# Optimization experiments

Hardware: AMD Instinct MI355X
Metric: run time of the kernel (lower is better)

## Reference

```python
import jax, jax.numpy as jnp
import numpy as np

D_HEAD = 128
N_HEADS = 8
BATCH = 8
SEQ = 1024


def setup_inputs() -> dict:
    key = jax.random.key(0)
    ks = jax.random.split(key, 11)
    d, nh = D_HEAD, N_HEADS
    D = nh * d
    s_in = 1.0 / np.sqrt(d)   # torch Linear default init bound, fan_in=d
    s_out = 1.0 / np.sqrt(D)  # fan_in=D for out_proj
    u = lambda k, shape, s: jax.random.uniform(k, shape, jnp.float32, -s, s)
    return {
        "q": jax.random.normal(ks[0], (BATCH, SEQ, d), jnp.float32),
        "k": jax.random.normal(ks[1], (BATCH, SEQ, d), jnp.float32),
        "v": jax.random.normal(ks[2], (BATCH, SEQ, d), jnp.float32),
        "Wq": u(ks[3], (d, D), s_in), "bq": u(ks[4], (D,), s_in),
        "Wk": u(ks[5], (d, D), s_in), "bk": u(ks[6], (D,), s_in),
        "Wv": u(ks[7], (d, D), s_in), "bv": u(ks[8], (D,), s_in),
        "Wo": u(ks[9], (D, d), s_out), "bo": u(ks[10], (d,), s_out),
    }


def reference(q, k, v, Wq, bq, Wk, bk, Wv, bv, Wo, bo):
    B, T, d_in = q.shape
    S = k.shape[1]
    nh = N_HEADS
    # projections: [B, L, nh*d] -> [B, nh, L, d]
    split = lambda x: x.reshape(x.shape[0], x.shape[1], nh, -1).transpose(0, 2, 1, 3)
    qh = split(q @ Wq + bq)
    kh = split(k @ Wk + bk)
    vh = split(v @ Wv + bv)
    d_head = qh.shape[-1]
    # scaled dot-product scores: [B, nh, T, S]
    scores = jnp.einsum('bhtd,bhsd->bhts', qh, kh) / jnp.sqrt(jnp.float32(d_head))
    # causal mask (future positions -> -inf), matches triu(fill(-inf), 1)
    causal = jnp.triu(jnp.ones((T, S), dtype=bool), 1)
    scores = jnp.where(causal[None, None], -jnp.inf, scores)
    # softmax in float32 then cast back, as the original does
    probs = jax.nn.softmax(scores.astype(jnp.float32), axis=-1).astype(scores.dtype)
    o = jnp.einsum('bhts,bhsd->bhtd', probs, vh)          # [B, nh, T, d]
    o = o.transpose(0, 2, 1, 3).reshape(B, T, nh * d_head)  # [B, T, D]
    return o @ Wo + bo                                     # [B, T, d]
```

## Files before the change

### kernel.cpp

```cpp
#include <hip/hip_runtime.h>
#include <hip/hip_bf16.h>


typedef __attribute__((ext_vector_type(8))) short short8;
typedef __attribute__((ext_vector_type(4))) short short4v;
typedef __attribute__((ext_vector_type(4))) float f32x4;

#define B_   8
#define S_   1024
#define DH_  128
#define NH_  8
#define DM_  1024

#define MFMA16(a, b, c) __builtin_amdgcn_mfma_f32_16x16x32_bf16((a), (b), (c), 0, 0, 0)

#define GLOAD_LDS16(gsrc, ldst)                                              \
  __builtin_amdgcn_global_load_lds(                                          \
      (const __attribute__((address_space(1))) void*)(gsrc),                 \
      (__attribute__((address_space(3))) void*)(ldst), 16, 0, 0)

__device__ __forceinline__ float bf2f(unsigned short u) {
  union { unsigned int i; float f; } x; x.i = ((unsigned int)u) << 16; return x.f;
}
__device__ __forceinline__ unsigned short f2bf(float f) {
  union { float f; unsigned int i; } x; x.f = f;
  unsigned int r = (x.i + 0x7fffu + ((x.i >> 16) & 1u)) >> 16;
  return (unsigned short)r;
}
__device__ __forceinline__ unsigned short f2h(float f) {
  union { _Float16 h; unsigned short u; } x; x.h = (_Float16)f; return x.u;
}
__device__ __forceinline__ float h2f(unsigned short u) {
  union { unsigned short u; _Float16 h; } x; x.u = u; return (float)x.h;
}
__device__ __forceinline__ float ldany(const void* p, int i, int fp) {
  return fp ? ((const float*)p)[i] : bf2f(((const unsigned short*)p)[i]);
}

__global__ void k_detect(const unsigned short* __restrict__ in, int* __restrict__ flag) {
  __shared__ int f;
  int tid = threadIdx.x;
  if (tid == 0) f = 0;
  __syncthreads();
  int t = 0;
  for (int i = tid; i < 16384; i += 256) {
    unsigned h = in[i];
    unsigned e = (h >> 7) & 0xFFu, m = h & 0x7Fu;
    if (e == 0xFFu || (e == 0u && m != 0u)) t = 1;
  }
  if (t) atomicOr(&f, 1);
  __syncthreads();
  if (tid == 0) *flag = f;
}

__global__ void k_cvt_x(const void* __restrict__ q, const void* __restrict__ k,
                        const void* __restrict__ v, const int* __restrict__ flag,
                        unsigned short* __restrict__ Xq, unsigned short* __restrict__ Xk,
                        unsigned short* __restrict__ Xv) {
  const int fp = *flag;
  int z = blockIdx.y;
  const void* in = (z == 0) ? q : (z == 1) ? k : v;
  unsigned short* out = (z == 0) ? Xq : (z == 1) ? Xk : Xv;
  int e8 = (blockIdx.x * 256 + threadIdx.x) * 8;
  if (fp) {
    const float* xf = (const float*)in + e8;
    f32x4 x0 = *(const f32x4*)xf;
    f32x4 x1 = *(const f32x4*)(xf + 4);
    short8 o;
#pragma unroll
    for (int j = 0; j < 4; ++j) { o[j] = (short)f2bf(x0[j]); o[4 + j] = (short)f2bf(x1[j]); }
    *(short8*)&out[e8] = o;
  } else {
    *(short8*)&out[e8] = *(const short8*)((const unsigned short*)in + e8);
  }
}

__global__ void k_cvt_w(const void* __restrict__ Wq, const void* __restrict__ Wk,
                        const void* __restrict__ Wv, const void* __restrict__ Wo,
                        const void* __restrict__ bq, const void* __restrict__ bk,
                        const void* __restrict__ bv, const void* __restrict__ bo,
                        const int* __restrict__ flag,
                        unsigned short* __restrict__ wqT, unsigned short* __restrict__ wkT,
                        unsigned short* __restrict__ wvT, unsigned short* __restrict__ woT,
                        unsigned short* __restrict__ bqc, unsigned short* __restrict__ bkc,
                        unsigned short* __restrict__ bvc, unsigned short* __restrict__ boc) {
  const int fp = *flag;
  int g = blockIdx.x * 256 + threadIdx.x;
  if (g < 393216) {
    int z = g >> 17, e = g & 131071;
    const void* in = (z == 0) ? Wq : (z == 1) ? Wk : Wv;
    unsigned short* out = (z == 0) ? wqT : (z == 1) ? wkT : wvT;
    int r = e >> 10, c = e & 1023;
    out[c * 128 + r] = f2bf(ldany(in, e, fp));
  } else if (g < 524288) {
    int e = g - 393216;
    int r = e >> 7, c = e & 127;
    woT[c * 1024 + r] = f2bf(ldany(Wo, e, fp));
  } else if (g < 525312) {
    int e = g - 524288; bqc[e] = f2bf(ldany(bq, e, fp));
  } else if (g < 526336) {
    int e = g - 525312; bkc[e] = f2bf(ldany(bk, e, fp));
  } else if (g < 527360) {
    int e = g - 526336; bvc[e] = f2bf(ldany(bv, e, fp));
  } else if (g < 527488) {
    int e = g - 527360; boc[e] = f2bf(ldany(bo, e, fp));
  }
}

__global__ __launch_bounds__(256) void k_qkv(
    const unsigned short* __restrict__ Xq, const unsigned short* __restrict__ Xk,
    const unsigned short* __restrict__ Xv,
    const unsigned short* __restrict__ WqT, const unsigned short* __restrict__ WkT,
    const unsigned short* __restrict__ WvT,
    const unsigned short* __restrict__ bq, const unsigned short* __restrict__ bk,
    const unsigned short* __restrict__ bv,
    unsigned short* __restrict__ Qp, unsigned short* __restrict__ Kp,
    unsigned short* __restrict__ VpT) {
  __shared__ __align__(16) unsigned short vtile[128][136];

  const int mat = blockIdx.z;
  const unsigned short* X    = (mat == 0) ? Xq  : (mat == 1) ? Xk  : Xv;
  const unsigned short* WT   = (mat == 0) ? WqT : (mat == 1) ? WkT : WvT;
  const unsigned short* bias = (mat == 0) ? bq  : (mat == 1) ? bk  : bv;
  const float scale = (mat == 0) ? (1.4426950408889634f / 11.313708498984761f) : 1.0f;

  const int tid = threadIdx.x, lane = tid & 63, wave = tid >> 6;
  const int wm = wave >> 1, wn = wave & 1;
  const int l15 = lane & 15, lg = lane >> 4;
  const int mbase = blockIdx.x * 128 + wm * 64;
  const int nbase = blockIdx.y * 128 + wn * 64;

  short8 a[4][4];
#pragma unroll
  for (int mi = 0; mi < 4; ++mi)
#pragma unroll
    for (int kk = 0; kk < 4; ++kk)
      a[mi][kk] = *(const short8*)&X[(mbase + mi * 16 + l15) * DH_ + kk * 32 + lg * 8];

  f32x4 acc[4][4];
#pragma unroll
  for (int mi = 0; mi < 4; ++mi)
#pragma unroll
    for (int ni = 0; ni < 4; ++ni) acc[mi][ni] = (f32x4){0.f, 0.f, 0.f, 0.f};

  short8 bfr[2][4];
#pragma unroll
  for (int kk = 0; kk < 4; ++kk)
    bfr[0][kk] = *(const short8*)&WT[(nbase + l15) * DH_ + kk * 32 + lg * 8];

#pragma unroll
  for (int ni = 0; ni < 4; ++ni) {
    if (ni < 3) {
#pragma unroll
      for (int kk = 0; kk < 4; ++kk)
        bfr[(ni + 1) & 1][kk] =
            *(const short8*)&WT[(nbase + (ni + 1) * 16 + l15) * DH_ + kk * 32 + lg * 8];
    }
#pragma unroll
    for (int mi = 0; mi < 4; ++mi)
#pragma unroll
      for (int kk = 0; kk < 4; ++kk)
        acc[mi][ni] = MFMA16(a[mi][kk], bfr[ni & 1][kk], acc[mi][ni]);
  }

#pragma unroll
  for (int mi = 0; mi < 4; ++mi)
#pragma unroll
    for (int ni = 0; ni < 4; ++ni) {
      int nl = wn * 64 + ni * 16 + l15;
      float bv_ = bf2f(bias[blockIdx.y * 128 + nl]);
#pragma unroll
      for (int reg = 0; reg < 4; ++reg) {
        int ml_ = wm * 64 + mi * 16 + lg * 4 + reg;
        vtile[ml_][nl] = f2bf((acc[mi][ni][reg] + bv_) * scale);
      }
    }
  __syncthreads();

  const int b = blockIdx.x >> 3;
  const int h = blockIdx.y;
  if (mat < 2) {
    unsigned short* Out = ((mat == 0) ? Qp : Kp) +
        ((b * NH_ + h) * S_ + (blockIdx.x & 7) * 128) * DH_;
#pragma unroll
    for (int j = 0; j < 8; ++j) {
      int r = j * 16 + (tid >> 4);
      int c0 = (tid & 15) * 8;
      short8 v = *(const short8*)&vtile[r][c0];
      *(short8*)&Out[j * 2048 + tid * 8] = v;
    }
  } else {
    int n = tid >> 1;
    int thalf = (tid & 1) * 64;
    int base = ((b * NH_ + h) * DH_ + n) * S_ + (blockIdx.x & 7) * 128 + thalf;
#pragma unroll
    for (int jj = 0; jj < 8; ++jj) {
      short8 v;
#pragma unroll
      for (int j2 = 0; j2 < 8; ++j2) v[j2] = (short)vtile[thalf + jj * 8 + j2][n];
      *(short8*)&VpT[base + jj * 8] = v;
    }
  }
}

__global__ __launch_bounds__(256) void k_attn_split(
    const unsigned short* __restrict__ Qp, const unsigned short* __restrict__ Kp,
    const unsigned short* __restrict__ VpT,
    unsigned short* __restrict__ Opart, float* __restrict__ ml,
    unsigned short* __restrict__ O) {
  __shared__ __align__(16) unsigned short kbuf[2][4096];
  __shared__ __align__(16) unsigned short vbuf[2][4096];
  __shared__ __align__(16) unsigned short plds[4][16][44];

  const int tid = threadIdx.x, lane = tid & 63, w = tid >> 6;
  const int l15 = lane & 15, lg = lane >> 4;

  const int bid = blockIdx.x;
  const int swz = (bid & 7) * 320 + (bid >> 3);
  const int bh = swz / 40;
  const int bj = 39 - (swz % 40);
  int G, c;
  if (bj < 4)       { G = bj;                  c = 0; }
  else if (bj < 12) { G = 4 + ((bj - 4) >> 1); c = (bj - 4) & 1; }
  else if (bj < 24) { G = 8 + (bj - 12) / 3;   c = (bj - 12) % 3; }
  else              { G = 12 + ((bj - 24) >> 2); c = (bj - 24) & 3; }
  const int qw = 4 * G + w;
  const int q0 = qw * 16;
  const int cd = G >> 2;
  const bool dia = (c == cd);
  const int sbeg = c * 256;
  const int nt_w   = dia ? ((qw >> 1) + 1 - 8 * c) : 8;
  const int nt_blk = dia ? (2 * G + 2 - 8 * c) : 8;

  const unsigned short* Qb = Qp + bh * (S_ * DH_);
  const unsigned short* Kb = Kp + bh * (S_ * DH_);
  const unsigned short* Vb = VpT + bh * (DH_ * S_);

  const int krow4 = lane >> 4;
  const int kslot = lane & 15;
  const int vd16  = lane >> 2;
  const int vslot = lane & 3;
  const int vsw   = vslot ^ ((vd16 >> 1) & 3);

#define STAGE(bb, sb_) do {                                                        \
    int r0_ = w * 8 + krow4;                                                       \
    GLOAD_LDS16(Kb + ((sb_) + r0_) * DH_ + ((kslot ^ (r0_ & 7)) * 8),              \
                &kbuf[bb][(w * 8) * 128]);                                         \
    int r1_ = w * 8 + 4 + krow4;                                                   \
    GLOAD_LDS16(Kb + ((sb_) + r1_) * DH_ + ((kslot ^ (r1_ & 7)) * 8),              \
                &kbuf[bb][(w * 8 + 4) * 128]);                                     \
    int d0_ = w * 32 + vd16;                                                       \
    GLOAD_LDS16(Vb + d0_ * S_ + (sb_) + vsw * 8, &vbuf[bb][(w * 32) * 32]);        \
    int d1_ = w * 32 + 16 + vd16;                                                  \
    GLOAD_LDS16(Vb + d1_ * S_ + (sb_) + vsw * 8, &vbuf[bb][(w * 32 + 16) * 32]);   \
  } while (0)

  short8 qf[4];
#pragma unroll
  for (int kk = 0; kk < 4; ++kk)
    qf[kk] = *(const short8*)&Qb[(q0 + l15) * DH_ + kk * 32 + lg * 8];

  short8 ones;
#pragma unroll
  for (int jj = 0; jj < 8; ++jj) ones[jj] = (short)0x3F80;

  f32x4 of[8], l_acc;
  float m_[4];
#pragma unroll
  for (int di = 0; di < 8; ++di) of[di] = (f32x4){0.f, 0.f, 0.f, 0.f};
  l_acc = (f32x4){0.f, 0.f, 0.f, 0.f};
#pragma unroll
  for (int reg = 0; reg < 4; ++reg) m_[reg] = -1e30f;

  STAGE(0, sbeg);
  __syncthreads();

  const int vrd = lg ^ ((l15 >> 1) & 3);
  for (int kt = 0; kt < nt_blk; ++kt) {
    const int cb = kt & 1;
    if (kt + 1 < nt_blk) STAGE(cb ^ 1, sbeg + (kt + 1) * 32);

    if (kt < nt_w) {
      const int sb = sbeg + kt * 32;
      const int xsl = l15 & 7;

      f32x4 s0 = (f32x4){0.f, 0.f, 0.f, 0.f}, s1 = (f32x4){0.f, 0.f, 0.f, 0.f};
#pragma unroll
      for (int kk = 0; kk < 4; ++kk) {
        short8 kf0 = *(const short8*)&kbuf[cb][l15 * 128 + (((kk * 4 + lg) ^ xsl) * 8)];
        short8 kf1 = *(const short8*)&kbuf[cb][(16 + l15) * 128 + (((kk * 4 + lg) ^ xsl) * 8)];
        s0 = MFMA16(qf[kk], kf0, s0);
        s1 = MFMA16(qf[kk], kf1, s1);
      }

      if (dia && kt == nt_w - 1) {
        const int qrow = q0 + lg * 4;
#pragma unroll
        for (int reg = 0; reg < 4; ++reg) {
          if (sb + l15 > qrow + reg)      s0[reg] = -1e30f;
          if (sb + 16 + l15 > qrow + reg) s1[reg] = -1e30f;
        }
      }

      bool need = false;
      float vmax[4];
#pragma unroll
      for (int reg = 0; reg < 4; ++reg) {
        vmax[reg] = fmaxf(s0[reg], s1[reg]);
        need |= (vmax[reg] > m_[reg] + 8.0f);
      }
      if (__any(need)) {
        float alpha[4];
#pragma unroll
        for (int reg = 0; reg < 4; ++reg) {
          float rm = vmax[reg];
#pragma unroll
          for (int d = 1; d < 16; d <<= 1) rm = fmaxf(rm, __shfl_xor(rm, d));
          float mn = fmaxf(m_[reg], rm);
          alpha[reg] = __builtin_amdgcn_exp2f(m_[reg] - mn);
          m_[reg] = mn;
        }
#pragma unroll
        for (int di = 0; di < 8; ++di)
#pragma unroll
          for (int reg = 0; reg < 4; ++reg) of[di][reg] *= alpha[reg];
#pragma unroll
        for (int reg = 0; reg < 4; ++reg) l_acc[reg] *= alpha[reg];
      }

#pragma unroll
      for (int reg = 0; reg < 4; ++reg) {
        float p0 = __builtin_amdgcn_exp2f(s0[reg] - m_[reg]);
        float p1 = __builtin_amdgcn_exp2f(s1[reg] - m_[reg]);
        union { float f; unsigned int i; } u0, u1;
        u0.f = p0; u1.f = p1;
        plds[w][lg * 4 + reg][l15]      = (unsigned short)((u0.i + 0x8000u) >> 16);
        plds[w][lg * 4 + reg][16 + l15] = (unsigned short)((u1.i + 0x8000u) >> 16);
      }

      short8 pa = *(const short8*)&plds[w][l15][lg * 8];

#pragma unroll
      for (int di = 0; di < 8; ++di) {
        short8 vfd = *(const short8*)&vbuf[cb][(di * 16 + l15) * 32 + vrd * 8];
        of[di] = MFMA16(pa, vfd, of[di]);
      }
      l_acc = MFMA16(pa, ones, l_acc);
    }
    __syncthreads();
  }

  if (qw < 16) {
    const int b = bh >> 3, h = bh & 7;
#pragma unroll
    for (int reg = 0; reg < 4; ++reg) {
      int row = lg * 4 + reg;
      float inv = 1.0f / l_acc[reg];
      int qq = q0 + row;
#pragma unroll
      for (int di = 0; di < 8; ++di)
        O[(b * S_ + qq) * DM_ + h * DH_ + di * 16 + l15] = f2bf(of[di][reg] * inv);
    }
  } else {
    int runit;
    if (qw < 32)      runit = 16 + 2 * (qw - 16) + c;
    else if (qw < 48) runit = 48 + 3 * (qw - 32) + c;
    else              runit = 96 + 4 * (qw - 48) + c;
    const int g = bh * 160 + runit;
    unsigned short* op = Opart + g * 2048;
    float* mlg = ml + g * 32;
#pragma unroll
    for (int reg = 0; reg < 4; ++reg) {
      int row = lg * 4 + reg;
      float inv = 1.0f / l_acc[reg];
#pragma unroll
      for (int di = 0; di < 8; ++di)
        op[row * 128 + di * 16 + l15] = f2h(of[di][reg] * inv);
      if (l15 == 0) {
        mlg[row * 2]     = m_[reg];
        mlg[row * 2 + 1] = l_acc[reg];
      }
    }
  }
#undef STAGE
}

__global__ void k_combine(const unsigned short* __restrict__ Opart,
                          const float* __restrict__ ml,
                          unsigned short* __restrict__ O) {
  const int bh = blockIdx.x / 48, qw = 16 + blockIdx.x % 48;
  const int nc = (qw >> 4) + 1;
  const int rbase = (qw < 32) ? 16 + 2 * (qw - 16)
                  : (qw < 48) ? 48 + 3 * (qw - 32)
                              : 96 + 4 * (qw - 48);
  const int g0 = bh * 160 + rbase;
  const int tid = threadIdx.x;
  const int row = tid >> 4, d0 = (tid & 15) * 8;

  float m[4], l[4];
  float mx = -1e30f;
  for (int i = 0; i < nc; ++i) {
    m[i] = ml[(g0 + i) * 32 + row * 2];
    l[i] = ml[(g0 + i) * 32 + row * 2 + 1];
    mx = fmaxf(mx, m[i]);
  }
  float wt[4], wsum = 0.f;
  for (int i = 0; i < nc; ++i) { wt[i] = l[i] * exp2f(m[i] - mx); wsum += wt[i]; }
  float invw = 1.0f / wsum;

  float acc[8];
#pragma unroll
  for (int jj = 0; jj < 8; ++jj) acc[jj] = 0.f;
  for (int i = 0; i < nc; ++i) {
    short8 v = *(const short8*)&Opart[(g0 + i) * 2048 + row * 128 + d0];
    float wgt = wt[i];
#pragma unroll
    for (int jj = 0; jj < 8; ++jj) acc[jj] += wgt * h2f((unsigned short)v[jj]);
  }

  const int b = bh >> 3, h = bh & 7;
  const int qq = qw * 16 + row;
  short8 o;
#pragma unroll
  for (int jj = 0; jj < 8; ++jj) o[jj] = (short)f2bf(acc[jj] * invw);
  *(short8*)&O[(b * S_ + qq) * DM_ + h * DH_ + d0] = o;
}

__global__ __launch_bounds__(256) void k_attn(
    const unsigned short* __restrict__ Qp, const unsigned short* __restrict__ Kp,
    const unsigned short* __restrict__ VpT, unsigned short* __restrict__ O) {
  __shared__ __align__(16) unsigned short plds[4][2][16][44];

  const int qt = 7 - blockIdx.x;
  const int bh = blockIdx.y;
  const int tid = threadIdx.x, lane = tid & 63, w = tid >> 6;
  const int l15 = lane & 15, lg = lane >> 4;
  const int q0 = qt * 128 + w * 32;

  const unsigned short* Qb = Qp + bh * (S_ * DH_);
  const unsigned short* Kb = Kp + bh * (S_ * DH_);
  const unsigned short* Vb = VpT + bh * (DH_ * S_);

  short8 qf[2][4];
#pragma unroll
  for (int mi = 0; mi < 2; ++mi)
#pragma unroll
    for (int kk = 0; kk < 4; ++kk)
      qf[mi][kk] = *(const short8*)&Qb[(q0 + mi * 16 + l15) * DH_ + kk * 32 + lg * 8];

  f32x4 of[2][8];
  float m_[2][4], l_[2][4];
#pragma unroll
  for (int mi = 0; mi < 2; ++mi) {
#pragma unroll
    for (int di = 0; di < 8; ++di) of[mi][di] = (f32x4){0.f, 0.f, 0.f, 0.f};
#pragma unroll
    for (int reg = 0; reg < 4; ++reg) { m_[mi][reg] = -1e30f; l_[mi][reg] = 0.f; }
  }

  const int ntiles = q0 / 32 + 1;
  for (int kt = 0; kt < ntiles; ++kt) {
    const int sb = kt * 32;
    const bool lastt = (kt == ntiles - 1);

    f32x4 s[2][2];
#pragma unroll
    for (int mi = 0; mi < 2; ++mi)
#pragma unroll
      for (int ni = 0; ni < 2; ++ni) s[mi][ni] = (f32x4){0.f, 0.f, 0.f, 0.f};
#pragma unroll
    for (int ni = 0; ni < 2; ++ni) {
      short8 kf[4];
#pragma unroll
      for (int kk = 0; kk < 4; ++kk)
        kf[kk] = *(const short8*)&Kb[(sb + ni * 16 + l15) * DH_ + kk * 32 + lg * 8];
#pragma unroll
      for (int mi = 0; mi < 2; ++mi)
#pragma unroll
        for (int kk = 0; kk < 4; ++kk)
          s[mi][ni] = MFMA16(qf[mi][kk], kf[kk], s[mi][ni]);
    }

#pragma unroll
    for (int mi = 0; mi < 2; ++mi) {
      float alpha[4];
#pragma unroll
      for (int reg = 0; reg < 4; ++reg) {
        int q = q0 + mi * 16 + lg * 4 + reg;
        float v0 = s[mi][0][reg];
        float v1 = s[mi][1][reg];
        if (lastt) {
          if (sb + l15 > q)      v0 = -1e30f;
          if (sb + 16 + l15 > q) v1 = -1e30f;
        }
        float rmax = fmaxf(v0, v1);
#pragma unroll
        for (int d = 1; d < 16; d <<= 1) rmax = fmaxf(rmax, __shfl_xor(rmax, d));
        float mn = fmaxf(m_[mi][reg], rmax);
        alpha[reg] = __builtin_amdgcn_exp2f(m_[mi][reg] - mn);
        m_[mi][reg] = mn;
        float p0 = __builtin_amdgcn_exp2f(v0 - mn), p1 = __builtin_amdgcn_exp2f(v1 - mn);
        float rs = p0 + p1;
#pragma unroll
        for (int d = 1; d < 16; d <<= 1) rs += __shfl_xor(rs, d);
        l_[mi][reg] = l_[mi][reg] * alpha[reg] + rs;
        plds[w][mi][lg * 4 + reg][l15]      = f2bf(p0);
        plds[w][mi][lg * 4 + reg][16 + l15] = f2bf(p1);
      }
#pragma unroll
      for (int di = 0; di < 8; ++di)
#pragma unroll
        for (int reg = 0; reg < 4; ++reg) of[mi][di][reg] *= alpha[reg];
    }

    short8 pa[2];
#pragma unroll
    for (int mi = 0; mi < 2; ++mi)
      pa[mi] = *(const short8*)&plds[w][mi][l15][lg * 8];

#pragma unroll
    for (int di = 0; di < 8; ++di) {
      short8 vf = *(const short8*)&Vb[(di * 16 + l15) * S_ + sb + lg * 8];
#pragma unroll
      for (int mi = 0; mi < 2; ++mi) of[mi][di] = MFMA16(pa[mi], vf, of[mi][di]);
    }
  }

  const int b = bh >> 3, h = bh & 7;
#pragma unroll
  for (int mi = 0; mi < 2; ++mi)
#pragma unroll
    for (int reg = 0; reg < 4; ++reg) {
      float inv = 1.0f / l_[mi][reg];
      int q = q0 + mi * 16 + lg * 4 + reg;
#pragma unroll
      for (int di = 0; di < 8; ++di) {
        int d = di * 16 + l15;
        O[(b * S_ + q) * DM_ + h * DH_ + d] = f2bf(of[mi][di][reg] * inv);
      }
    }
}

__global__ __launch_bounds__(256) void k_oproj(
    const unsigned short* __restrict__ O, const unsigned short* __restrict__ WoT,
    const unsigned short* __restrict__ boc, const int* __restrict__ flag,
    void* __restrict__ out) {
  const int tid = threadIdx.x, lane = tid & 63, w = tid >> 6;
  const int l15 = lane & 15, lg = lane >> 4;
  const int mrow = blockIdx.x * 16;

  f32x4 acc[2];
  acc[0] = (f32x4){0.f, 0.f, 0.f, 0.f};
  acc[1] = (f32x4){0.f, 0.f, 0.f, 0.f};

#pragma unroll 2
  for (int ks = 0; ks < 32; ++ks) {
    int kb = ks * 32;
    short8 a  = *(const short8*)&O[(mrow + l15) * DM_ + kb + lg * 8];
    short8 b0 = *(const short8*)&WoT[(w * 32 + l15) * DM_ + kb + lg * 8];
    short8 b1 = *(const short8*)&WoT[(w * 32 + 16 + l15) * DM_ + kb + lg * 8];
    acc[0] = MFMA16(a, b0, acc[0]);
    acc[1] = MFMA16(a, b1, acc[1]);
  }

  const int fp = *flag;
#pragma unroll
  for (int ni = 0; ni < 2; ++ni) {
    int n = w * 32 + ni * 16 + l15;
    float bv_ = bf2f(boc[n]);
#pragma unroll
    for (int reg = 0; reg < 4; ++reg) {
      int m = mrow + lg * 4 + reg;
      float val = acc[ni][reg] + bv_;
      if (fp) ((float*)out)[m * 128 + n] = val;
      else    ((unsigned short*)out)[m * 128 + n] = f2bf(val);
    }
  }
}

extern "C" void kernel_launch(void* const* d_in, const int* in_sizes, int n_in,
                              void* d_out, int out_size, void* d_ws, size_t ws_size,
                              hipStream_t stream) {
  const void* q  = d_in[0];
  const void* k  = d_in[1];
  const void* v  = d_in[2];
  const void* Wq = d_in[3];
  const void* bq = d_in[4];
  const void* Wk = d_in[5];
  const void* bk = d_in[6];
  const void* Wv = d_in[7];
  const void* bv = d_in[8];
  const void* Wo = d_in[9];
  const void* bo = d_in[10];

  char* ws = (char*)d_ws;
  int*            flag = (int*)(ws + 0);
  unsigned short* wqT  = (unsigned short*)(ws + 4096);
  unsigned short* wkT  = (unsigned short*)(ws + 266240);
  unsigned short* wvT  = (unsigned short*)(ws + 528384);
  unsigned short* woT  = (unsigned short*)(ws + 790528);
  unsigned short* bqc  = (unsigned short*)(ws + 1052672);
  unsigned short* bkc  = (unsigned short*)(ws + 1054720);
  unsigned short* bvc  = (unsigned short*)(ws + 1056768);
  unsigned short* boc  = (unsigned short*)(ws + 1058816);
  unsigned short* Xq   = (unsigned short*)(ws + 2097152);
  unsigned short* Xk   = (unsigned short*)(ws + 4194304);
  unsigned short* Xv   = (unsigned short*)(ws + 6291456);
  float*          ml   = (float*)(ws + 2097152);
  unsigned short* Qp   = (unsigned short*)(ws + 8388608);
  unsigned short* Kp   = (unsigned short*)(ws + 25165824);
  unsigned short* VpT  = (unsigned short*)(ws + 41943040);
  unsigned short* O    = (unsigned short*)(ws + 58720256);
  unsigned short* Opart= (unsigned short*)(ws + 75497472);

  const bool use_split = ws_size >= (size_t)117440512;

  k_detect<<<dim3(1), 256, 0, stream>>>((const unsigned short*)q, flag);
  k_cvt_x<<<dim3(512, 3), 256, 0, stream>>>(q, k, v, flag, Xq, Xk, Xv);
  k_cvt_w<<<dim3(2061), 256, 0, stream>>>(Wq, Wk, Wv, Wo, bq, bk, bv, bo, flag,
                                          wqT, wkT, wvT, woT, bqc, bkc, bvc, boc);
  k_qkv<<<dim3(64, 8, 3), 256, 0, stream>>>(Xq, Xk, Xv, wqT, wkT, wvT, bqc, bkc, bvc,
                                            Qp, Kp, VpT);
  if (use_split) {
    k_attn_split<<<dim3(2560), 256, 0, stream>>>(Qp, Kp, VpT, Opart, ml, O);
    k_combine<<<dim3(3072), 256, 0, stream>>>(Opart, ml, O);
  } else {
    k_attn<<<dim3(8, 64), 256, 0, stream>>>(Qp, Kp, VpT, O);
  }
  k_oproj<<<dim3(512), 256, 0, stream>>>(O, woT, boc, flag, d_out);
}
```

Baseline: 151.7 us.

## Coarsen attention KV split to 512-key chunks and split out-proj over N

The split-KV attention now uses chunks of 512 keys, so each query group gets at most two partial results instead of up to four. That cuts the attention blocks from 2560 to 1536 and the combine blocks from 3072 to 2048, and simplifies the combine into a fixed two-way merge. This lowers partial-result traffic and combine work, but each block does longer serial loops and the grid has fewer blocks to balance. The output projection is also split across two grid columns, with each wave computing one 16-column tile instead of two, to double the block count. The cost is loading the O tile twice.

```diff
diff --git a/kernel.cpp b/kernel.cpp
--- a/kernel.cpp
+++ b/kernel.cpp
@@ -216,21 +216,20 @@
   const int l15 = lane & 15, lg = lane >> 4;
 
   const int bid = blockIdx.x;
-  const int swz = (bid & 7) * 320 + (bid >> 3);
-  const int bh = swz / 40;
-  const int bj = 39 - (swz % 40);
+  const int swz = (bid & 7) * 192 + (bid >> 3);
+  const int bh = swz / 24;
+  const int bj = swz % 24;
   int G, c;
-  if (bj < 4)       { G = bj;                  c = 0; }
-  else if (bj < 12) { G = 4 + ((bj - 4) >> 1); c = (bj - 4) & 1; }
-  else if (bj < 24) { G = 8 + (bj - 12) / 3;   c = (bj - 12) % 3; }
-  else              { G = 12 + ((bj - 24) >> 2); c = (bj - 24) & 3; }
+  if (bj < 8)       { G = 8 + bj;        c = 0; }
+  else if (bj < 16) { G = 15 - bj;       c = 0; }
+  else              { G = 8 + (23 - bj); c = 1; }
   const int qw = 4 * G + w;
   const int q0 = qw * 16;
-  const int cd = G >> 2;
+  const int cd = G >> 3;
   const bool dia = (c == cd);
-  const int sbeg = c * 256;
-  const int nt_w   = dia ? ((qw >> 1) + 1 - 8 * c) : 8;
-  const int nt_blk = dia ? (2 * G + 2 - 8 * c) : 8;
+  const int sbeg = c * 512;
+  const int nt_w   = dia ? ((qw >> 1) + 1 - 16 * c) : 16;
+  const int nt_blk = dia ? (2 * G + 2 - 16 * c) : 16;
 
   const unsigned short* Qb = Qp + bh * (S_ * DH_);
   const unsigned short* Kb = Kp + bh * (S_ * DH_);
@@ -350,7 +349,7 @@
     __syncthreads();
   }
 
-  if (qw < 16) {
+  if (qw < 32) {
     const int b = bh >> 3, h = bh & 7;
 #pragma unroll
     for (int reg = 0; reg < 4; ++reg) {
@@ -362,11 +361,7 @@
         O[(b * S_ + qq) * DM_ + h * DH_ + di * 16 + l15] = f2bf(of[di][reg] * inv);
     }
   } else {
-    int runit;
-    if (qw < 32)      runit = 16 + 2 * (qw - 16) + c;
-    else if (qw < 48) runit = 48 + 3 * (qw - 32) + c;
-    else              runit = 96 + 4 * (qw - 48) + c;
-    const int g = bh * 160 + runit;
+    const int g = bh * 64 + 2 * (qw - 32) + c;
     unsigned short* op = Opart + g * 2048;
     float* mlg = ml + g * 32;
 #pragma unroll
@@ -388,41 +383,28 @@
 __global__ void k_combine(const unsigned short* __restrict__ Opart,
                           const float* __restrict__ ml,
                           unsigned short* __restrict__ O) {
-  const int bh = blockIdx.x / 48, qw = 16 + blockIdx.x % 48;
-  const int nc = (qw >> 4) + 1;
-  const int rbase = (qw < 32) ? 16 + 2 * (qw - 16)
-                  : (qw < 48) ? 48 + 3 * (qw - 32)
-                              : 96 + 4 * (qw - 48);
-  const int g0 = bh * 160 + rbase;
+  const int bh = blockIdx.x >> 5, qw = 32 + (blockIdx.x & 31);
+  const int g0 = bh * 64 + 2 * (qw - 32);
   const int tid = threadIdx.x;
   const int row = tid >> 4, d0 = (tid & 15) * 8;
 
-  float m[4], l[4];
-  float mx = -1e30f;
-  for (int i = 0; i < nc; ++i) {
-    m[i] = ml[(g0 + i) * 32 + row * 2];
-    l[i] = ml[(g0 + i) * 32 + row * 2 + 1];
-    mx = fmaxf(mx, m[i]);
-  }
-  float wt[4], wsum = 0.f;
-  for (int i = 0; i < nc; ++i) { wt[i] = l[i] * exp2f(m[i] - mx); wsum += wt[i]; }
-  float invw = 1.0f / wsum;
-
-  float acc[8];
-#pragma unroll
-  for (int jj = 0; jj < 8; ++jj) acc[jj] = 0.f;
-  for (int i = 0; i < nc; ++i) {
-    short8 v = *(const short8*)&Opart[(g0 + i) * 2048 + row * 128 + d0];
-    float wgt = wt[i];
-#pragma unroll
-    for (int jj = 0; jj < 8; ++jj) acc[jj] += wgt * h2f((unsigned short)v[jj]);
-  }
+  float m0 = ml[g0 * 32 + row * 2],       l0 = ml[g0 * 32 + row * 2 + 1];
+  float m1 = ml[(g0 + 1) * 32 + row * 2], l1 = ml[(g0 + 1) * 32 + row * 2 + 1];
+  float mx = fmaxf(m0, m1);
+  float w0 = l0 * exp2f(m0 - mx), w1 = l1 * exp2f(m1 - mx);
+  float invw = 1.0f / (w0 + w1);
+
+  short8 v0 = *(const short8*)&Opart[g0 * 2048 + row * 128 + d0];
+  short8 v1 = *(const short8*)&Opart[(g0 + 1) * 2048 + row * 128 + d0];
 
   const int b = bh >> 3, h = bh & 7;
   const int qq = qw * 16 + row;
   short8 o;
 #pragma unroll
-  for (int jj = 0; jj < 8; ++jj) o[jj] = (short)f2bf(acc[jj] * invw);
+  for (int jj = 0; jj < 8; ++jj) {
+    float acc = w0 * h2f((unsigned short)v0[jj]) + w1 * h2f((unsigned short)v1[jj]);
+    o[jj] = (short)f2bf(acc * invw);
+  }
   *(short8*)&O[(b * S_ + qq) * DM_ + h * DH_ + d0] = o;
 }
 
@@ -548,33 +530,27 @@
   const int tid = threadIdx.x, lane = tid & 63, w = tid >> 6;
   const int l15 = lane & 15, lg = lane >> 4;
   const int mrow = blockIdx.x * 16;
-
-  f32x4 acc[2];
-  acc[0] = (f32x4){0.f, 0.f, 0.f, 0.f};
-  acc[1] = (f32x4){0.f, 0.f, 0.f, 0.f};
-
-#pragma unroll 2
+  const int nbase = blockIdx.y * 64 + w * 16;
+
+  f32x4 acc = (f32x4){0.f, 0.f, 0.f, 0.f};
+
+#pragma unroll 4
   for (int ks = 0; ks < 32; ++ks) {
     int kb = ks * 32;
-    short8 a  = *(const short8*)&O[(mrow + l15) * DM_ + kb + lg * 8];
-    short8 b0 = *(const short8*)&WoT[(w * 32 + l15) * DM_ + kb + lg * 8];
-    short8 b1 = *(const short8*)&WoT[(w * 32 + 16 + l15) * DM_ + kb + lg * 8];
-    acc[0] = MFMA16(a, b0, acc[0]);
-    acc[1] = MFMA16(a, b1, acc[1]);
+    short8 a = *(const short8*)&O[(mrow + l15) * DM_ + kb + lg * 8];
+    short8 b = *(const short8*)&WoT[(nbase + l15) * DM_ + kb + lg * 8];
+    acc = MFMA16(a, b, acc);
   }
 
   const int fp = *flag;
-#pragma unroll
-  for (int ni = 0; ni < 2; ++ni) {
-    int n = w * 32 + ni * 16 + l15;
-    float bv_ = bf2f(boc[n]);
-#pragma unroll
-    for (int reg = 0; reg < 4; ++reg) {
-      int m = mrow + lg * 4 + reg;
-      float val = acc[ni][reg] + bv_;
-      if (fp) ((float*)out)[m * 128 + n] = val;
-      else    ((unsigned short*)out)[m * 128 + n] = f2bf(val);
-    }
+  const int n = nbase + l15;
+  const float bv_ = bf2f(boc[n]);
+#pragma unroll
+  for (int reg = 0; reg < 4; ++reg) {
+    int m = mrow + lg * 4 + reg;
+    float val = acc[reg] + bv_;
+    if (fp) ((float*)out)[m * 128 + n] = val;
+    else    ((unsigned short*)out)[m * 128 + n] = f2bf(val);
   }
 }
 
@@ -622,10 +598,10 @@
   k_qkv<<<dim3(64, 8, 3), 256, 0, stream>>>(Xq, Xk, Xv, wqT, wkT, wvT, bqc, bkc, bvc,
                                             Qp, Kp, VpT);
   if (use_split) {
-    k_attn_split<<<dim3(2560), 256, 0, stream>>>(Qp, Kp, VpT, Opart, ml, O);
-    k_combine<<<dim3(3072), 256, 0, stream>>>(Opart, ml, O);
+    k_attn_split<<<dim3(1536), 256, 0, stream>>>(Qp, Kp, VpT, Opart, ml, O);
+    k_combine<<<dim3(2048), 256, 0, stream>>>(Opart, ml, O);
   } else {
     k_attn<<<dim3(8, 64), 256, 0, stream>>>(Qp, Kp, VpT, O);
   }
-  k_oproj<<<dim3(512), 256, 0, stream>>>(O, woT, boc, flag, d_out);
-}
+  k_oproj<<<dim3(512, 2), 256, 0, stream>>>(O, woT, boc, flag, d_out);
+}
```

Measured after the change: 153.9 us. Within noise of the previous version (+1.4%).
